# Kernel optimization log

Measured on AMD Instinct MI355X. Metric: run time of the kernel, lower is better.

## Reference

```python
import jax, jax.numpy as jnp
import numpy as np

B, S, D, H, F, V, K = 8, 1024, 1024, 16, 4096, 8192, 64
HD = D // H
ALPHA = 0.1


def layernorm(x, g, b, eps=1e-5):
    mu = jnp.mean(x, axis=-1, keepdims=True)
    var = jnp.var(x, axis=-1, keepdims=True)
    return (x - mu) * jax.lax.rsqrt(var + eps) * g + b


def setup_inputs() -> dict:
    key = jax.random.key(0)
    ks = jax.random.split(key, 16)
    s = lambda fan: 1.0 / np.sqrt(fan)
    inp = {
        "x": jax.random.normal(ks[0], (B, S, D), jnp.float32),
        "token_ids": jax.random.randint(ks[1], (B, S), 0, V),
        "pmi": jax.random.normal(ks[2], (V, V), jnp.float32) * 0.1,
        "Wq": jax.random.normal(ks[3], (D, D), jnp.float32) * s(D),
        "bq": jnp.zeros((D,), jnp.float32),
        "Wk": jax.random.normal(ks[4], (D, D), jnp.float32) * s(D),
        "bk": jnp.zeros((D,), jnp.float32),
        "Wv": jax.random.normal(ks[5], (D, D), jnp.float32) * s(D),
        "bv": jnp.zeros((D,), jnp.float32),
        "Wo": jax.random.normal(ks[6], (D, D), jnp.float32) * s(D),
        "bo": jnp.zeros((D,), jnp.float32),
        "W1": jax.random.normal(ks[7], (D, F), jnp.float32) * s(D),
        "b1": jnp.zeros((F,), jnp.float32),
        "W2": jax.random.normal(ks[8], (F, D), jnp.float32) * s(F),
        "b2": jnp.zeros((D,), jnp.float32),
        "g1": jnp.ones((D,), jnp.float32),
        "be1": jnp.zeros((D,), jnp.float32),
        "g2": jnp.ones((D,), jnp.float32),
        "be2": jnp.zeros((D,), jnp.float32),
    }
    return inp


def reference(x, token_ids, pmi, Wq, bq, Wk, bk, Wv, bv, Wo, bo,
              W1, b1, W2, b2, g1, be1, g2, be2):
    # --- SparseStatAttention: QK^T + alpha*PMI bias, top-k mask, softmax ---
    q = (x @ Wq + bq).reshape(B, S, H, HD)
    k = (x @ Wk + bk).reshape(B, S, H, HD)
    v = (x @ Wv + bv).reshape(B, S, H, HD)
    scores = jnp.einsum("bihd,bjhd->bhij", q, k) / np.sqrt(HD)  # [B,H,S,S]
    bias = pmi[token_ids[:, :, None], token_ids[:, None, :]]     # [B,S,S]
    scores = scores + ALPHA * bias[:, None, :, :]
    # top-k sparsification per query row (threshold at k-th largest value)
    kth = jax.lax.top_k(scores, K)[0][..., -1:]
    scores = jnp.where(scores >= kth, scores, -jnp.inf)
    w = jax.nn.softmax(scores, axis=-1)
    attn = jnp.einsum("bhij,bjhd->bihd", w, v).reshape(B, S, D)
    attn = attn @ Wo + bo
    # --- residual + norm1 (dropout is identity in eval) ---
    h = layernorm(x + attn, g1, be1)
    # --- GELU FFN (torch nn.GELU default = exact erf) ---
    ff = jax.nn.gelu(h @ W1 + b1, approximate=False) @ W2 + b2
    return layernorm(h + ff, g2, be2)
```

## Files before the change

### kernel.cpp

```cpp
#include <hip/hip_runtime.h>
#include <cstdint>
#include <cstddef>

#define B_   8
#define S_   1024
#define D_   1024
#define H_   16
#define HD_  64
#define F_   4096
#define V_   8192
#define KTOP 64

typedef unsigned short ushort_t;
typedef __attribute__((ext_vector_type(8))) short short8;
typedef __attribute__((ext_vector_type(8))) _Float16 half8;
typedef __attribute__((ext_vector_type(4))) float floatx4;
typedef __attribute__((ext_vector_type(4))) unsigned int uintx4;
typedef __attribute__((ext_vector_type(4))) float floatv4;
typedef __attribute__((ext_vector_type(4))) unsigned short ushortx4;
typedef __attribute__((ext_vector_type(8))) unsigned short ushortx8;

__device__ __forceinline__ ushort_t f2bf(float f) {
    unsigned int u = __builtin_bit_cast(unsigned int, f);
    u += 0x7fffu + ((u >> 16) & 1u);
    return (ushort_t)(u >> 16);
}
__device__ __forceinline__ float bf2f(ushort_t u) {
    unsigned int x = ((unsigned int)u) << 16;
    return __builtin_bit_cast(float, x);
}
__device__ __forceinline__ ushort_t f2h(float f) {
    _Float16 h = (_Float16)f;
    return __builtin_bit_cast(ushort_t, h);
}
__device__ __forceinline__ float h2f(ushort_t u) {
    return (float)__builtin_bit_cast(_Float16, u);
}

__device__ __forceinline__ void gload_lds16(const ushort_t* g, ushort_t* lds_base) {
    __builtin_amdgcn_global_load_lds(
        (const __attribute__((address_space(1))) unsigned int*)g,
        (__attribute__((address_space(3))) unsigned int*)lds_base,
        16, 0, 0);
}

__global__ __launch_bounds__(256) void cast_x_kernel(const float* __restrict__ x,
                                                     ushort_t* __restrict__ xb) {
    int gid = blockIdx.x * 256 + threadIdx.x;
    floatv4 v = ((const floatv4*)x)[gid];
    ushortx4 o;
    o[0] = f2bf(v[0]); o[1] = f2bf(v[1]); o[2] = f2bf(v[2]); o[3] = f2bf(v[3]);
    ((ushortx4*)xb)[gid] = o;
}

__global__ void transpose_cast_kernel(const float* __restrict__ W, ushort_t* __restrict__ WT,
                                      int K, int N, float scale) {
    __shared__ float tile[32][33];
    int n0 = blockIdx.x * 32, k0 = blockIdx.y * 32;
    #pragma unroll
    for (int i = threadIdx.y; i < 32; i += 8)
        tile[i][threadIdx.x] = W[(size_t)(k0 + i) * N + n0 + threadIdx.x];
    __syncthreads();
    #pragma unroll
    for (int i = threadIdx.y; i < 32; i += 8)
        WT[(size_t)(n0 + i) * K + k0 + threadIdx.x] = f2bf(tile[threadIdx.x][i] * scale);
}

__global__ __launch_bounds__(256) void pack_bias3_kernel(const float* __restrict__ bq,
                                                         const float* __restrict__ bk,
                                                         const float* __restrict__ bv,
                                                         float* __restrict__ o) {
    int i = blockIdx.x * 256 + threadIdx.x;
    float v = (i < 1024) ? bq[i] * 0.125f : (i < 2048) ? bk[i - 1024] : bv[i - 2048];
    o[i] = v;
}

__global__ __launch_bounds__(256) void bias_gather_kernel(const int* __restrict__ tok,
                                                          const float* __restrict__ pmi,
                                                          ushort_t* __restrict__ biasb) {
    int b = blockIdx.x >> 10;
    int i = blockIdx.x & (S_ - 1);
    int ti = tok[b * S_ + i];
    const float* prow = pmi + (size_t)ti * V_;
    #pragma unroll
    for (int it = 0; it < 4; it++) {
        int j = threadIdx.x + it * 256;
        int tj = tok[b * S_ + j];
        biasb[(size_t)blockIdx.x * S_ + j] = f2h(0.1f * prow[tj]);
    }
}

__global__ __launch_bounds__(256) void transpose_v_kernel(const ushort_t* __restrict__ v,
                                                          ushort_t* __restrict__ vT) {
    __shared__ ushort_t t[64 * 72];
    int bh = blockIdx.x >> 4;
    int s0 = (blockIdx.x & 15) * 64;
    #pragma unroll
    for (int it = 0; it < 2; it++) {
        int idx = threadIdx.x + it * 256;
        int sl = idx >> 3, dg = (idx & 7) * 8;
        *(uintx4*)&t[sl * 72 + dg] = *(const uintx4*)&v[((size_t)bh * S_ + s0 + sl) * HD_ + dg];
    }
    __syncthreads();
    #pragma unroll
    for (int it = 0; it < 2; it++) {
        int idx = threadIdx.x + it * 256;
        int dl = idx >> 3, sg = (idx & 7) * 8;
        ushortx8 o;
        #pragma unroll
        for (int i = 0; i < 8; i++) o[i] = f2h(bf2f(t[(sg + i) * 72 + dl]));
        *(ushortx8*)&vT[((size_t)bh * HD_ + dl) * S_ + s0 + sg] = o;
    }
}

__global__ __launch_bounds__(256) void gemm_bt(const ushort_t* __restrict__ A,
                                               const ushort_t* __restrict__ BT,
                                               const float* __restrict__ bias,
                                               ushort_t* __restrict__ C,
                                               int M, int N, int K, int ep) {
    __shared__ ushort_t As[128 * 32];
    __shared__ ushort_t Bs[128 * 32];

    const int tid = threadIdx.x;
    const int wid = tid >> 6, lane = tid & 63;
    const int quad = lane >> 4, r = lane & 15;
    const int wr = wid >> 1, wc = wid & 1;
    const int m0 = blockIdx.y * 128, n0 = blockIdx.x * 128;

    floatx4 acc[4][4];
    #pragma unroll
    for (int a = 0; a < 4; a++)
        #pragma unroll
        for (int b = 0; b < 4; b++) acc[a][b] = (floatx4){0.f, 0.f, 0.f, 0.f};

    const int srow = wid * 16 + (lane >> 2);
    const int scol = (lane & 3) * 8;
    const ushort_t* Ag0 = A + (size_t)(m0 + srow) * K + scol;
    const ushort_t* Ag1 = A + (size_t)(m0 + 64 + srow) * K + scol;
    const ushort_t* Bg0 = BT + (size_t)(n0 + srow) * K + scol;
    const ushort_t* Bg1 = BT + (size_t)(n0 + 64 + srow) * K + scol;
    ushort_t* Asd0 = As + (wid * 16) * 32;
    ushort_t* Asd1 = As + (64 + wid * 16) * 32;
    ushort_t* Bsd0 = Bs + (wid * 16) * 32;
    ushort_t* Bsd1 = Bs + (64 + wid * 16) * 32;

    for (int k0 = 0; k0 < K; k0 += 32) {
        __syncthreads();
        gload_lds16(Ag0 + k0, Asd0);
        gload_lds16(Ag1 + k0, Asd1);
        gload_lds16(Bg0 + k0, Bsd0);
        gload_lds16(Bg1 + k0, Bsd1);
        __syncthreads();

        short8 af[4], bf[4];
        #pragma unroll
        for (int t = 0; t < 4; t++)
            af[t] = *(const short8*)&As[(wr * 64 + t * 16 + r) * 32 + quad * 8];
        #pragma unroll
        for (int t = 0; t < 4; t++)
            bf[t] = *(const short8*)&Bs[(wc * 64 + t * 16 + r) * 32 + quad * 8];
        #pragma unroll
        for (int tm = 0; tm < 4; tm++)
            #pragma unroll
            for (int tn = 0; tn < 4; tn++)
                acc[tm][tn] = __builtin_amdgcn_mfma_f32_16x16x32_bf16(af[tm], bf[tn], acc[tm][tn], 0, 0, 0);
    }

    #pragma unroll
    for (int tm = 0; tm < 4; tm++) {
        #pragma unroll
        for (int tn = 0; tn < 4; tn++) {
            const int n = n0 + wc * 64 + tn * 16 + r;
            const float bv = bias[n];
            #pragma unroll
            for (int i2 = 0; i2 < 4; i2++) {
                const int m = m0 + wr * 64 + tm * 16 + quad * 4 + i2;
                float v = acc[tm][tn][i2] + bv;
                if (ep == 1) v = 0.5f * v * (1.0f + erff(v * 0.70710678118654752f));
                size_t idx;
                if (ep == 2) {
                    int tensor = n >> 10, nn = n & 1023;
                    idx = (size_t)tensor * (B_ * S_ * D_)
                        + (((size_t)(m >> 10) * H_ + (nn >> 6)) * S_ + (m & (S_ - 1))) * HD_ + (nn & (HD_ - 1));
                } else {
                    idx = (size_t)m * N + n;
                }
                C[idx] = f2bf(v);
            }
        }
    }
}

__global__ __launch_bounds__(256) void attn_kernel(const ushort_t* __restrict__ q,
                                                   const ushort_t* __restrict__ k,
                                                   const ushort_t* __restrict__ vT,
                                                   const ushort_t* __restrict__ biasb,
                                                   ushort_t* __restrict__ attnb) {
    extern __shared__ char smem[];
    ushort_t* q_lds = (ushort_t*)smem;
    ushort_t* Sm = (ushort_t*)(smem + 2304);
    _Float16* Smh = (_Float16*)Sm;
    const int SST = 1032;

    const int bid = blockIdx.x;
    const int b = bid >> 10;
    const int h = (bid >> 6) & (H_ - 1);
    const int i0 = (bid & 63) * 16;
    const int tid = threadIdx.x;
    const int wid = tid >> 6, lane = tid & 63;
    const int quad = lane >> 4, r = lane & 15;

    const size_t bh = (size_t)b * H_ + h;
    const ushort_t* qbase = q + bh * S_ * HD_;
    const ushort_t* kbase = k + bh * S_ * HD_;
    const ushort_t* vbase = vT + bh * HD_ * S_;
    const ushort_t* bsrc = biasb + ((size_t)b * S_ + i0) * S_;

    if (tid < 128) {
        int row = tid >> 3, dg = (tid & 7) * 8;
        *(uintx4*)&q_lds[row * 72 + dg] = *(const uintx4*)&qbase[(size_t)(i0 + row) * HD_ + dg];
    }
    #pragma unroll
    for (int c8 = 0; c8 < 8; c8++) {
        int c = wid * 8 + c8;
        int row = c >> 1, half = c & 1;
        gload_lds16(bsrc + (size_t)row * S_ + half * 512 + lane * 8,
                    Sm + row * SST + half * 512);
    }
    __syncthreads();

    short8 aq0 = *(const short8*)&q_lds[r * 72 + quad * 8];
    short8 aq1 = *(const short8*)&q_lds[r * 72 + 32 + quad * 8];
    #pragma unroll 4
    for (int t = 0; t < 16; t++) {
        int jt = (t * 4 + wid) * 16;
        floatx4 acc;
        #pragma unroll
        for (int i2 = 0; i2 < 4; i2++)
            acc[i2] = (float)Smh[(quad * 4 + i2) * SST + jt + r];
        const ushort_t* kp = kbase + (size_t)(jt + r) * HD_ + quad * 8;
        short8 b0 = *(const short8*)kp;
        short8 b1 = *(const short8*)(kp + 32);
        acc = __builtin_amdgcn_mfma_f32_16x16x32_bf16(aq0, b0, acc, 0, 0, 0);
        acc = __builtin_amdgcn_mfma_f32_16x16x32_bf16(aq1, b1, acc, 0, 0, 0);
        #pragma unroll
        for (int i2 = 0; i2 < 4; i2++)
            Smh[(quad * 4 + i2) * SST + jt + r] = (_Float16)acc[i2];
    }
    __syncthreads();

    for (int rr = 0; rr < 4; rr++) {
        int row = wid * 4 + rr;
        const ushort_t* Srow = Sm + row * SST;
        float sv[16]; unsigned int kk[16];
        float mx = -3.4e38f;
        #pragma unroll
        for (int t = 0; t < 16; t++) {
            unsigned int u = Srow[t * 64 + lane];
            sv[t] = h2f((ushort_t)u);
            kk[t] = (u & 0x8000u) ? (0xFFFFu & ~u) : (u | 0x8000u);
            mx = fmaxf(mx, sv[t]);
        }
        #pragma unroll
        for (int off = 32; off; off >>= 1) mx = fmaxf(mx, __shfl_xor(mx, off));
        unsigned int T = 0u;
        for (int bit = 15; bit >= 0; bit--) {
            unsigned int trial = T | (1u << bit);
            int c = 0;
            #pragma unroll
            for (int t = 0; t < 16; t++)
                c += __popcll(__ballot(kk[t] >= trial));
            if (c >= KTOP) T = trial;
        }
        float ev[16]; float sum = 0.f;
        #pragma unroll
        for (int t = 0; t < 16; t++) {
            ev[t] = (kk[t] >= T) ? __expf(sv[t] - mx) : 0.f;
            sum += ev[t];
        }
        #pragma unroll
        for (int off = 32; off; off >>= 1) sum += __shfl_xor(sum, off);
        float inv = 1.f / sum;
        ushort_t* wrow = (ushort_t*)Srow;
        #pragma unroll
        for (int t = 0; t < 16; t++) wrow[t * 64 + lane] = f2h(ev[t] * inv);
    }
    __syncthreads();

    floatx4 oacc = (floatx4){0.f, 0.f, 0.f, 0.f};
    for (int ks = 0; ks < 32; ks++) {
        half8 wa = *(const half8*)&Smh[r * SST + ks * 32 + quad * 8];
        half8 vbf = *(const half8*)&vbase[(size_t)(wid * 16 + r) * S_ + ks * 32 + quad * 8];
        oacc = __builtin_amdgcn_mfma_f32_16x16x32_f16(wa, vbf, oacc, 0, 0, 0);
    }
    #pragma unroll
    for (int i2 = 0; i2 < 4; i2++) {
        int row = quad * 4 + i2;
        attnb[((size_t)b * S_ + i0 + row) * D_ + h * HD_ + wid * 16 + r] = f2bf(oacc[i2]);
    }
}

__global__ __launch_bounds__(256) void ln1_kernel(const float* __restrict__ x,
                                                  const ushort_t* __restrict__ t,
                                                  const float* __restrict__ g,
                                                  const float* __restrict__ be,
                                                  ushort_t* __restrict__ hb) {
    int row = blockIdx.x, tid = threadIdx.x;
    const float* xr = x + (size_t)row * D_;
    const ushort_t* tr = t + (size_t)row * D_;
    float v[4]; float s = 0.f, s2 = 0.f;
    #pragma unroll
    for (int it = 0; it < 4; it++) {
        int j = tid + it * 256;
        v[it] = xr[j] + bf2f(tr[j]);
        s += v[it]; s2 += v[it] * v[it];
    }
    #pragma unroll
    for (int off = 32; off; off >>= 1) { s += __shfl_xor(s, off); s2 += __shfl_xor(s2, off); }
    __shared__ float rs[4], rq[4];
    if ((tid & 63) == 0) { rs[tid >> 6] = s; rq[tid >> 6] = s2; }
    __syncthreads();
    s = rs[0] + rs[1] + rs[2] + rs[3];
    s2 = rq[0] + rq[1] + rq[2] + rq[3];
    float mu = s * (1.f / D_);
    float var = s2 * (1.f / D_) - mu * mu;
    float rstd = rsqrtf(var + 1e-5f);
    #pragma unroll
    for (int it = 0; it < 4; it++) {
        int j = tid + it * 256;
        hb[(size_t)row * D_ + j] = f2bf((v[it] - mu) * rstd * g[j] + be[j]);
    }
}

__global__ __launch_bounds__(256) void ln2_kernel(const ushort_t* __restrict__ hbuf,
                                                  const ushort_t* __restrict__ t,
                                                  const float* __restrict__ g,
                                                  const float* __restrict__ be,
                                                  float* __restrict__ out) {
    int row = blockIdx.x, tid = threadIdx.x;
    const ushort_t* hr = hbuf + (size_t)row * D_;
    const ushort_t* tr = t + (size_t)row * D_;
    float v[4]; float s = 0.f, s2 = 0.f;
    #pragma unroll
    for (int it = 0; it < 4; it++) {
        int j = tid + it * 256;
        v[it] = bf2f(hr[j]) + bf2f(tr[j]);
        s += v[it]; s2 += v[it] * v[it];
    }
    #pragma unroll
    for (int off = 32; off; off >>= 1) { s += __shfl_xor(s, off); s2 += __shfl_xor(s2, off); }
    __shared__ float rs[4], rq[4];
    if ((tid & 63) == 0) { rs[tid >> 6] = s; rq[tid >> 6] = s2; }
    __syncthreads();
    s = rs[0] + rs[1] + rs[2] + rs[3];
    s2 = rq[0] + rq[1] + rq[2] + rq[3];
    float mu = s * (1.f / D_);
    float var = s2 * (1.f / D_) - mu * mu;
    float rstd = rsqrtf(var + 1e-5f);
    #pragma unroll
    for (int it = 0; it < 4; it++) {
        int j = tid + it * 256;
        out[(size_t)row * D_ + j] = (v[it] - mu) * rstd * g[j] + be[j];
    }
}

extern "C" void kernel_launch(void* const* d_in, const int* in_sizes, int n_in,
                              void* d_out, int out_size, void* d_ws, size_t ws_size,
                              hipStream_t stream) {
    (void)in_sizes; (void)n_in; (void)out_size; (void)ws_size;
    const float* x   = (const float*)d_in[0];
    const int*   tok = (const int*)d_in[1];
    const float* pmi = (const float*)d_in[2];
    const float* Wq  = (const float*)d_in[3];
    const float* bq  = (const float*)d_in[4];
    const float* Wk  = (const float*)d_in[5];
    const float* bk  = (const float*)d_in[6];
    const float* Wv  = (const float*)d_in[7];
    const float* bv  = (const float*)d_in[8];
    const float* Wo  = (const float*)d_in[9];
    const float* bo  = (const float*)d_in[10];
    const float* W1  = (const float*)d_in[11];
    const float* b1  = (const float*)d_in[12];
    const float* W2  = (const float*)d_in[13];
    const float* b2  = (const float*)d_in[14];
    const float* g1  = (const float*)d_in[15];
    const float* be1 = (const float*)d_in[16];
    const float* g2  = (const float*)d_in[17];
    const float* be2 = (const float*)d_in[18];
    float* out = (float*)d_out;

    char* ws = (char*)d_ws;
    size_t off = 0;
    auto alloc = [&](size_t bytes) { char* p = ws + off; off += (bytes + 255) & ~(size_t)255; return p; };
    const size_t BSD = (size_t)B_ * S_ * D_;
    ushort_t* xb     = (ushort_t*)alloc(BSD * 2);
    ushort_t* WqkvT  = (ushort_t*)alloc((size_t)3 * D_ * D_ * 2);
    ushort_t* WoT    = (ushort_t*)alloc((size_t)D_ * D_ * 2);
    ushort_t* W1T    = (ushort_t*)alloc((size_t)D_ * F_ * 2);
    ushort_t* W2T    = (ushort_t*)alloc((size_t)F_ * D_ * 2);
    float*    bqkv   = (float*)alloc(3072 * 4);
    ushort_t* qkvb   = (ushort_t*)alloc(3 * BSD * 2);
    ushort_t* vT     = (ushort_t*)alloc(BSD * 2);
    ushort_t* biasb  = (ushort_t*)alloc((size_t)B_ * S_ * S_ * 2);
    ushort_t* extra  = (ushort_t*)alloc(BSD * 2);
    (void)extra;
    ushort_t* qb    = qkvb;
    ushort_t* kb    = qkvb + BSD;
    ushort_t* vb    = qkvb + 2 * BSD;
    ushort_t* attnb = xb;
    ushort_t* tbuf  = qb;
    ushort_t* hb    = kb;
    ushort_t* ffb   = vb;

    const size_t attn_lds = 2304 + 16 * 1032 * 2;

    cast_x_kernel<<<8192, 256, 0, stream>>>(x, xb);
    transpose_cast_kernel<<<dim3(32, 32), dim3(32, 8), 0, stream>>>(Wq, WqkvT, D_, D_, 0.125f);
    transpose_cast_kernel<<<dim3(32, 32), dim3(32, 8), 0, stream>>>(Wk, WqkvT + (size_t)D_ * D_, D_, D_, 1.0f);
    transpose_cast_kernel<<<dim3(32, 32), dim3(32, 8), 0, stream>>>(Wv, WqkvT + (size_t)2 * D_ * D_, D_, D_, 1.0f);
    transpose_cast_kernel<<<dim3(32, 32), dim3(32, 8), 0, stream>>>(Wo, WoT, D_, D_, 1.0f);
    transpose_cast_kernel<<<dim3(128, 32), dim3(32, 8), 0, stream>>>(W1, W1T, D_, F_, 1.0f);
    transpose_cast_kernel<<<dim3(32, 128), dim3(32, 8), 0, stream>>>(W2, W2T, F_, D_, 1.0f);
    pack_bias3_kernel<<<12, 256, 0, stream>>>(bq, bk, bv, bqkv);
    bias_gather_kernel<<<B_ * S_, 256, 0, stream>>>(tok, pmi, biasb);

    gemm_bt<<<dim3(24, 64), 256, 0, stream>>>(xb, WqkvT, bqkv, qkvb, B_ * S_, 3 * D_, D_, 2);
    transpose_v_kernel<<<B_ * H_ * (S_ / 64), 256, 0, stream>>>(vb, vT);

    attn_kernel<<<B_ * H_ * (S_ / 16), 256, attn_lds, stream>>>(qb, kb, vT, biasb, attnb);

    gemm_bt<<<dim3(8, 64), 256, 0, stream>>>(attnb, WoT, bo, tbuf, B_ * S_, D_, D_, 0);
    ln1_kernel<<<B_ * S_, 256, 0, stream>>>(x, tbuf, g1, be1, hb);
    gemm_bt<<<dim3(32, 64), 256, 0, stream>>>(hb, W1T, b1, ffb, B_ * S_, F_, D_, 1);
    gemm_bt<<<dim3(8, 64), 256, 0, stream>>>(ffb, W2T, b2, tbuf, B_ * S_, D_, F_, 0);
    ln2_kernel<<<B_ * S_, 256, 0, stream>>>(hb, tbuf, g2, be2, out);
}
```

Measured before the change: 1.179 ms.

## Swizzle attention score tile in LDS and narrow the top-k radix search

Replaces the padded score tile in LDS with an XOR-swizzled 1024-stride layout, so the per-row softmax can use 16-byte vector LDS reads and writes without bank conflicts, and drops the LDS copy of Q in favour of direct global loads. The top-k bitwise threshold search now starts at the highest bit where the row max and the minimum of per-lane maxima differ, and exits early once exactly K elements pass. The PV loop uses two independent MFMA accumulators to shorten the dependency chain. The changes add index arithmetic, and the swizzle must agree across the gather, QK, softmax and PV stages.

```diff
diff --git a/kernel.cpp b/kernel.cpp
--- a/kernel.cpp
+++ b/kernel.cpp
@@ -197,10 +197,8 @@
                                                    const ushort_t* __restrict__ biasb,
                                                    ushort_t* __restrict__ attnb) {
     extern __shared__ char smem[];
-    ushort_t* q_lds = (ushort_t*)smem;
-    ushort_t* Sm = (ushort_t*)(smem + 2304);
-    _Float16* Smh = (_Float16*)Sm;
-    const int SST = 1032;
+    ushort_t* Sm = (ushort_t*)smem;
+    _Float16* Smh = (_Float16*)smem;
 
     const int bid = blockIdx.x;
     const int b = bid >> 10;
@@ -216,28 +214,31 @@
     const ushort_t* vbase = vT + bh * HD_ * S_;
     const ushort_t* bsrc = biasb + ((size_t)b * S_ + i0) * S_;
 
-    if (tid < 128) {
-        int row = tid >> 3, dg = (tid & 7) * 8;
-        *(uintx4*)&q_lds[row * 72 + dg] = *(const uintx4*)&qbase[(size_t)(i0 + row) * HD_ + dg];
-    }
     #pragma unroll
     for (int c8 = 0; c8 < 8; c8++) {
         int c = wid * 8 + c8;
         int row = c >> 1, half = c & 1;
-        gload_lds16(bsrc + (size_t)row * S_ + half * 512 + lane * 8,
-                    Sm + row * SST + half * 512);
-    }
-    __syncthreads();
-
-    short8 aq0 = *(const short8*)&q_lds[r * 72 + quad * 8];
-    short8 aq1 = *(const short8*)&q_lds[r * 72 + 32 + quad * 8];
+        int xr = row & 7;
+        gload_lds16(bsrc + (size_t)row * S_ + half * 512 + (lane ^ xr) * 8,
+                    Sm + row * 1024 + half * 512);
+    }
+    short8 aq0 = *(const short8*)&qbase[(size_t)(i0 + r) * HD_ + quad * 8];
+    short8 aq1 = *(const short8*)&qbase[(size_t)(i0 + r) * HD_ + 32 + quad * 8];
+    __syncthreads();
+
     #pragma unroll 4
     for (int t = 0; t < 16; t++) {
         int jt = (t * 4 + wid) * 16;
+        int cb = (jt + r) >> 3;
+        int co = r & 7;
         floatx4 acc;
-        #pragma unroll
-        for (int i2 = 0; i2 < 4; i2++)
-            acc[i2] = (float)Smh[(quad * 4 + i2) * SST + jt + r];
+        int la[4];
+        #pragma unroll
+        for (int i2 = 0; i2 < 4; i2++) {
+            int row = quad * 4 + i2;
+            la[i2] = row * 1024 + ((cb ^ (row & 7)) << 3) + co;
+            acc[i2] = (float)Smh[la[i2]];
+        }
         const ushort_t* kp = kbase + (size_t)(jt + r) * HD_ + quad * 8;
         short8 b0 = *(const short8*)kp;
         short8 b1 = *(const short8*)(kp + 32);
@@ -245,54 +246,91 @@
         acc = __builtin_amdgcn_mfma_f32_16x16x32_bf16(aq1, b1, acc, 0, 0, 0);
         #pragma unroll
         for (int i2 = 0; i2 < 4; i2++)
-            Smh[(quad * 4 + i2) * SST + jt + r] = (_Float16)acc[i2];
+            Smh[la[i2]] = (_Float16)acc[i2];
     }
     __syncthreads();
 
     for (int rr = 0; rr < 4; rr++) {
         int row = wid * 4 + rr;
-        const ushort_t* Srow = Sm + row * SST;
-        float sv[16]; unsigned int kk[16];
-        float mx = -3.4e38f;
-        #pragma unroll
-        for (int t = 0; t < 16; t++) {
-            unsigned int u = Srow[t * 64 + lane];
-            sv[t] = h2f((ushort_t)u);
-            kk[t] = (u & 0x8000u) ? (0xFFFFu & ~u) : (u | 0x8000u);
-            mx = fmaxf(mx, sv[t]);
-        }
-        #pragma unroll
-        for (int off = 32; off; off >>= 1) mx = fmaxf(mx, __shfl_xor(mx, off));
-        unsigned int T = 0u;
-        for (int bit = 15; bit >= 0; bit--) {
+        ushort_t* Srow = Sm + row * 1024;
+        ushortx8 u0 = *(const ushortx8*)&Srow[lane * 8];
+        ushortx8 u1 = *(const ushortx8*)&Srow[(64 + lane) * 8];
+        unsigned int kk[16];
+        unsigned int lmax = 0u;
+        #pragma unroll
+        for (int t = 0; t < 8; t++) {
+            unsigned int ua = u0[t];
+            kk[t] = ua ^ ((ua & 0x8000u) ? 0xFFFFu : 0x8000u);
+            lmax = kk[t] > lmax ? kk[t] : lmax;
+            unsigned int ub = u1[t];
+            kk[8 + t] = ub ^ ((ub & 0x8000u) ? 0xFFFFu : 0x8000u);
+            lmax = kk[8 + t] > lmax ? kk[8 + t] : lmax;
+        }
+        unsigned int M = lmax, T0 = lmax;
+        #pragma unroll
+        for (int off = 32; off; off >>= 1) {
+            unsigned int om = (unsigned int)__shfl_xor((int)M, off);
+            unsigned int ot = (unsigned int)__shfl_xor((int)T0, off);
+            M = om > M ? om : M;
+            T0 = ot < T0 ? ot : T0;
+        }
+        float mx = h2f((ushort_t)((M & 0x8000u) ? (M ^ 0x8000u) : (~M & 0xFFFFu)));
+        unsigned int T;
+        int hb;
+        unsigned int diff = T0 ^ M;
+        if (diff == 0u) { T = M; hb = -1; }
+        else { hb = 31 - __builtin_clz(diff); T = M & ~((2u << hb) - 1u); }
+        for (int bit = hb; bit >= 0; bit--) {
             unsigned int trial = T | (1u << bit);
             int c = 0;
             #pragma unroll
             for (int t = 0; t < 16; t++)
                 c += __popcll(__ballot(kk[t] >= trial));
-            if (c >= KTOP) T = trial;
+            if (c >= KTOP) {
+                T = trial;
+                if (c == KTOP) break;
+            }
         }
         float ev[16]; float sum = 0.f;
         #pragma unroll
-        for (int t = 0; t < 16; t++) {
-            ev[t] = (kk[t] >= T) ? __expf(sv[t] - mx) : 0.f;
-            sum += ev[t];
+        for (int t = 0; t < 8; t++) {
+            float sa = h2f((ushort_t)u0[t]);
+            float ea = (kk[t] >= T) ? __expf(sa - mx) : 0.f;
+            ev[t] = ea; sum += ea;
+            float sb = h2f((ushort_t)u1[t]);
+            float eb = (kk[8 + t] >= T) ? __expf(sb - mx) : 0.f;
+            ev[8 + t] = eb; sum += eb;
         }
         #pragma unroll
         for (int off = 32; off; off >>= 1) sum += __shfl_xor(sum, off);
         float inv = 1.f / sum;
-        ushort_t* wrow = (ushort_t*)Srow;
-        #pragma unroll
-        for (int t = 0; t < 16; t++) wrow[t * 64 + lane] = f2h(ev[t] * inv);
-    }
-    __syncthreads();
-
-    floatx4 oacc = (floatx4){0.f, 0.f, 0.f, 0.f};
-    for (int ks = 0; ks < 32; ks++) {
-        half8 wa = *(const half8*)&Smh[r * SST + ks * 32 + quad * 8];
-        half8 vbf = *(const half8*)&vbase[(size_t)(wid * 16 + r) * S_ + ks * 32 + quad * 8];
-        oacc = __builtin_amdgcn_mfma_f32_16x16x32_f16(wa, vbf, oacc, 0, 0, 0);
-    }
+        ushortx8 w0, w1;
+        #pragma unroll
+        for (int t = 0; t < 8; t++) {
+            w0[t] = f2h(ev[t] * inv);
+            w1[t] = f2h(ev[8 + t] * inv);
+        }
+        *(ushortx8*)&Srow[lane * 8] = w0;
+        *(ushortx8*)&Srow[(64 + lane) * 8] = w1;
+    }
+    __syncthreads();
+
+    floatx4 o0 = (floatx4){0.f, 0.f, 0.f, 0.f};
+    floatx4 o1 = (floatx4){0.f, 0.f, 0.f, 0.f};
+    const _Float16* Srowp = Smh + (size_t)r * 1024;
+    const int xr = r & 7;
+    const ushort_t* vrow = vbase + (size_t)(wid * 16 + r) * S_;
+    #pragma unroll 4
+    for (int ks2 = 0; ks2 < 16; ks2++) {
+        int ks = ks2 * 2;
+        half8 wa0 = *(const half8*)&Srowp[((ks * 4 + quad) ^ xr) << 3];
+        half8 wa1 = *(const half8*)&Srowp[(((ks + 1) * 4 + quad) ^ xr) << 3];
+        half8 vb0 = *(const half8*)&vrow[ks * 32 + quad * 8];
+        half8 vb1 = *(const half8*)&vrow[(ks + 1) * 32 + quad * 8];
+        o0 = __builtin_amdgcn_mfma_f32_16x16x32_f16(wa0, vb0, o0, 0, 0, 0);
+        o1 = __builtin_amdgcn_mfma_f32_16x16x32_f16(wa1, vb1, o1, 0, 0, 0);
+    }
+    floatx4 oacc = o0 + o1;
     #pragma unroll
     for (int i2 = 0; i2 < 4; i2++) {
         int row = quad * 4 + i2;
@@ -412,7 +450,7 @@
     ushort_t* hb    = kb;
     ushort_t* ffb   = vb;
 
-    const size_t attn_lds = 2304 + 16 * 1032 * 2;
+    const size_t attn_lds = 16 * 1024 * 2;
 
     cast_x_kernel<<<8192, 256, 0, stream>>>(x, xb);
     transpose_cast_kernel<<<dim3(32, 32), dim3(32, 8), 0, stream>>>(Wq, WqkvT, D_, D_, 0.125f);
```

New measurement: 1.148 ms. -2.6%, faster.
